# Performance work log

Hardware: AMD Instinct MI355X
Metric: run time of the kernel (lower is better)

The kernel has to match this reference:

```python
import jax, jax.numpy as jnp
import numpy as np

EMBED_DIM = 1024
NUM_HEADS = 16
HEAD_DIM = EMBED_DIM // NUM_HEADS


def setup_inputs() -> dict:
    key = jax.random.key(0)
    k1, k2, k3 = jax.random.split(key, 3)
    B, S = 2, 2048
    x = jax.random.normal(k1, (B, S, EMBED_DIM), dtype=jnp.float32)
    # Xavier-uniform-style init for dense kernels
    lim_qkv = float(np.sqrt(6.0 / (EMBED_DIM + 3 * EMBED_DIM)))
    w_qkv = jax.random.uniform(k2, (EMBED_DIM, 3 * EMBED_DIM), jnp.float32, -lim_qkv, lim_qkv)
    b_qkv = jnp.zeros((3 * EMBED_DIM,), jnp.float32)
    lim_out = float(np.sqrt(6.0 / (EMBED_DIM + EMBED_DIM)))
    w_out = jax.random.uniform(k3, (EMBED_DIM, EMBED_DIM), jnp.float32, -lim_out, lim_out)
    b_out = jnp.zeros((EMBED_DIM,), jnp.float32)
    return {"x": x, "w_qkv": w_qkv, "b_qkv": b_qkv, "w_out": w_out, "b_out": b_out}


def reference(x, w_qkv, b_qkv, w_out, b_out):
    B, S, E = x.shape
    qkv = x @ w_qkv + b_qkv                       # [B, S, 3E]
    qkv = qkv.reshape(B, S, NUM_HEADS, 3 * HEAD_DIM)
    qkv = qkv.transpose(0, 2, 1, 3)               # [B, H, S, 3*dh]
    q, k, v = jnp.split(qkv, 3, axis=-1)          # each [B, H, S, dh]
    scale = 1.0 / jnp.sqrt(jnp.asarray(HEAD_DIM, x.dtype))
    logits = jnp.einsum('bhqd,bhkd->bhqk', q, k) * scale  # [B, H, S, S]
    attn = jax.nn.softmax(logits, axis=-1)
    vals = jnp.einsum('bhqk,bhkd->bhqd', attn, v)  # [B, H, S, dh]
    vals = vals.transpose(0, 2, 1, 3).reshape(B, S, E)
    return vals @ w_out + b_out
```

## Files before the change

### kernel.cpp

```cpp
#include <hip/hip_runtime.h>
#include <cstdint>

typedef unsigned short u16;
typedef unsigned int u32;
typedef __attribute__((ext_vector_type(8))) short bf16x8;
typedef __attribute__((ext_vector_type(4))) float f32x4;

#if __has_builtin(__builtin_amdgcn_exp2f)
#define EXP2(x) __builtin_amdgcn_exp2f(x)
#else
#define EXP2(x) exp2f(x)
#endif

__device__ __forceinline__ u16 f2bf(float f) {
  unsigned u = __float_as_uint(f);
  u += 0x7fffu + ((u >> 16) & 1u);
  return (u16)(u >> 16);
}
__device__ __forceinline__ u32 pk_bf16(float lo, float hi) {
#if __has_builtin(__builtin_amdgcn_cvt_pk_bf16_f32)
  auto r = __builtin_amdgcn_cvt_pk_bf16_f32(lo, hi);
  return __builtin_bit_cast(u32, r);
#else
  u32 a = __float_as_uint(lo), b = __float_as_uint(hi);
  a += 0x7fffu + ((a >> 16) & 1u);
  b += 0x7fffu + ((b >> 16) & 1u);
  return (a >> 16) | (b & 0xffff0000u);
#endif
}

__device__ __forceinline__ void async_load16(const void* g, void* l) {
  typedef const __attribute__((address_space(1))) void* gp_t;
  typedef __attribute__((address_space(3))) void* lp_t;
  __builtin_amdgcn_global_load_lds((gp_t)(uintptr_t)g, (lp_t)(uintptr_t)l, 16, 0, 0);
}

__global__ __launch_bounds__(256) void cvt_f32_bf16(
    const float* __restrict__ src, u16* __restrict__ dst)
{
  const size_t i = ((size_t)blockIdx.x * 256 + threadIdx.x) * 8;
  const float4 a = *(const float4*)(src + i);
  const float4 b = *(const float4*)(src + i + 4);
  union { u16 u[8]; bf16x8 v; } p;
  p.u[0] = f2bf(a.x); p.u[1] = f2bf(a.y); p.u[2] = f2bf(a.z); p.u[3] = f2bf(a.w);
  p.u[4] = f2bf(b.x); p.u[5] = f2bf(b.y); p.u[6] = f2bf(b.z); p.u[7] = f2bf(b.w);
  *(bf16x8*)(dst + i) = p.v;
}

__global__ __launch_bounds__(256) void transpose_cvt(
    const float* __restrict__ src, u16* __restrict__ dst, int rows, int cols)
{
  __shared__ u16 tile[64][65];
  const int t = threadIdx.x;
  const int r = t >> 2, c0 = (t & 3) * 16;
  const int tr = blockIdx.y * 64, tc = blockIdx.x * 64;
  const float* sp = src + (size_t)(tr + r) * cols + tc + c0;
#pragma unroll
  for (int i = 0; i < 16; i += 4) {
    const float4 v = *(const float4*)(sp + i);
    tile[r][c0 + i + 0] = f2bf(v.x);
    tile[r][c0 + i + 1] = f2bf(v.y);
    tile[r][c0 + i + 2] = f2bf(v.z);
    tile[r][c0 + i + 3] = f2bf(v.w);
  }
  __syncthreads();
  u16* dp = dst + (size_t)(tc + r) * rows + tr + c0;
#pragma unroll
  for (int i = 0; i < 16; ++i) dp[i] = tile[c0 + i][r];
}

__global__ __launch_bounds__(256) void transpose_v(
    const u16* __restrict__ src, u16* __restrict__ dst)
{
  __shared__ u16 tile[64][72];
  const int t = threadIdx.x;
  const int r = t >> 2, c0 = (t & 3) * 16;
  const int bh = blockIdx.y, s0 = blockIdx.x * 64;
  const u16* sp = src + ((size_t)bh * 2048 + s0 + r) * 64 + c0;
  union { u16 u[8]; bf16x8 v; } a, b;
  a.v = *(const bf16x8*)sp;
  b.v = *(const bf16x8*)(sp + 8);
#pragma unroll
  for (int i = 0; i < 8; ++i) tile[r][c0 + i] = a.u[i];
#pragma unroll
  for (int i = 0; i < 8; ++i) tile[r][c0 + 8 + i] = b.u[i];
  __syncthreads();
  union { u16 u[8]; bf16x8 v; } x, y;
#pragma unroll
  for (int i = 0; i < 8; ++i) x.u[i] = tile[c0 + i][r];
#pragma unroll
  for (int i = 0; i < 8; ++i) y.u[i] = tile[c0 + 8 + i][r];
  u16* dp = dst + ((size_t)bh * 64 + r) * 2048 + s0 + c0;
  *(bf16x8*)dp = x.v;
  *(bf16x8*)(dp + 8) = y.v;
}

__global__ __launch_bounds__(256) void gemm_qkv(
    const u16* __restrict__ A, const u16* __restrict__ Bt, const float* __restrict__ bias,
    u16* __restrict__ Qp, u16* __restrict__ Kp, u16* __restrict__ Vp, int Kd)
{
  __shared__ __align__(16) u16 As[128 * 32];
  __shared__ __align__(16) u16 Bs[128 * 32];
  const int t = threadIdx.x;
  const int lane = t & 63, wave = t >> 6;
  const int quad = lane >> 4, m16 = lane & 15;
  const int mb = blockIdx.y * 128, nb = blockIdx.x * 128;
  const int wr = (wave & 1) * 64, wc = (wave >> 1) * 64;

  const int srow = t >> 2;
  const int scol = (t & 3) * 8;
  const u16* Ag0 = A + (size_t)(mb + srow) * Kd + scol;
  const u16* Ag1 = Ag0 + (size_t)64 * Kd;
  const u16* Bg0 = Bt + (size_t)(nb + srow) * Kd + scol;
  const u16* Bg1 = Bg0 + (size_t)64 * Kd;
  u16* AsD = As + t * 8;
  u16* BsD = Bs + t * 8;

  f32x4 acc[4][4] = {};

  for (int k0 = 0; k0 < Kd; k0 += 32) {
    __syncthreads();
    async_load16(Ag0 + k0, AsD);
    async_load16(Ag1 + k0, AsD + 2048);
    async_load16(Bg0 + k0, BsD);
    async_load16(Bg1 + k0, BsD + 2048);
    __syncthreads();
    bf16x8 af[4], bfr[4];
#pragma unroll
    for (int i = 0; i < 4; ++i)
      af[i] = *(const bf16x8*)(As + (wr + i * 16 + m16) * 32 + quad * 8);
#pragma unroll
    for (int i = 0; i < 4; ++i)
      bfr[i] = *(const bf16x8*)(Bs + (wc + i * 16 + m16) * 32 + quad * 8);
#pragma unroll
    for (int i = 0; i < 4; ++i)
#pragma unroll
      for (int j = 0; j < 4; ++j)
        acc[i][j] = __builtin_amdgcn_mfma_f32_16x16x32_bf16(af[i], bfr[j], acc[i][j], 0, 0, 0);
  }

#pragma unroll
  for (int j = 0; j < 4; ++j) {
    const int base = nb + wc + j * 16;
    const float bv = bias[base + m16];
    const int seg = base >> 6;
    const int h = seg / 3;
    const int which = seg - h * 3;
    const int d = (base & 63) + m16;
    const float qs = (which == 0) ? 0.18033688011112042f : 1.0f;
#pragma unroll
    for (int i = 0; i < 4; ++i)
#pragma unroll
      for (int r = 0; r < 4; ++r) {
        const int row = mb + wr + i * 16 + quad * 4 + r;
        const int b = row >> 11, sI = row & 2047;
        const u16 v = f2bf((acc[i][j][r] + bv) * qs);
        const size_t idx = (((size_t)((b << 4) | h)) * 2048 + sI) * 64 + d;
        if (which == 0)      Qp[idx] = v;
        else if (which == 1) Kp[idx] = v;
        else                 Vp[idx] = v;
      }
  }
}

__global__ __launch_bounds__(256) void gemm_out(
    const u16* __restrict__ A, const u16* __restrict__ Bt, const float* __restrict__ bias,
    float* __restrict__ Outp)
{
  const int Kd = 1024;
  __shared__ __align__(16) u16 As[64 * 32];
  __shared__ __align__(16) u16 Bs[128 * 32];
  const int t = threadIdx.x;
  const int lane = t & 63, wave = t >> 6;
  const int quad = lane >> 4, m16 = lane & 15;
  const int mb = blockIdx.y * 64, nb = blockIdx.x * 128;
  const int wr = (wave & 1) * 32, wc = (wave >> 1) * 64;

  const int srow = t >> 2;
  const int scol = (t & 3) * 8;
  const u16* Ag0 = A + (size_t)(mb + srow) * Kd + scol;
  const u16* Bg0 = Bt + (size_t)(nb + srow) * Kd + scol;
  const u16* Bg1 = Bg0 + (size_t)64 * Kd;
  u16* AsD = As + t * 8;
  u16* BsD = Bs + t * 8;

  f32x4 acc[2][4] = {};

  for (int k0 = 0; k0 < Kd; k0 += 32) {
    __syncthreads();
    async_load16(Ag0 + k0, AsD);
    async_load16(Bg0 + k0, BsD);
    async_load16(Bg1 + k0, BsD + 2048);
    __syncthreads();
    bf16x8 af[2], bfr[4];
#pragma unroll
    for (int i = 0; i < 2; ++i)
      af[i] = *(const bf16x8*)(As + (wr + i * 16 + m16) * 32 + quad * 8);
#pragma unroll
    for (int j = 0; j < 4; ++j)
      bfr[j] = *(const bf16x8*)(Bs + (wc + j * 16 + m16) * 32 + quad * 8);
#pragma unroll
    for (int i = 0; i < 2; ++i)
#pragma unroll
      for (int j = 0; j < 4; ++j)
        acc[i][j] = __builtin_amdgcn_mfma_f32_16x16x32_bf16(af[i], bfr[j], acc[i][j], 0, 0, 0);
  }

#pragma unroll
  for (int j = 0; j < 4; ++j) {
    const int col = nb + wc + j * 16 + m16;
    const float bv = bias[col];
#pragma unroll
    for (int i = 0; i < 2; ++i)
#pragma unroll
      for (int r = 0; r < 4; ++r) {
        const int row = mb + wr + i * 16 + quad * 4 + r;
        Outp[(size_t)row * 1024 + col] = acc[i][j][r] + bv;
      }
  }
}

__global__ __launch_bounds__(256) void flash_attn(
    const u16* __restrict__ Q, const u16* __restrict__ K, const u16* __restrict__ Vt,
    u16* __restrict__ O)
{
  const int S = 2048;
  __shared__ __align__(16) u16 Kl[2][64 * 64];
  __shared__ __align__(16) u16 Vl[2][64 * 64];
  __shared__ __align__(16) u32 Pl[4][16 * 32];
  const int t = threadIdx.x;
  const int lane = t & 63, w = t >> 6;
  const int quad = lane >> 4, m16 = lane & 15;

  const int f = blockIdx.x;
  const int wi = f >> 3;
  const int bh = (f & 7) + 8 * (wi & 3);
  const int q0 = (wi >> 2) * 64;

  const u16* Qb = Q + (size_t)bh * S * 64;
  const u16* Kb = K + (size_t)bh * S * 64;
  const u16* Vb = Vt + (size_t)bh * 64 * S;

  bf16x8 qf[2];
#pragma unroll
  for (int ks = 0; ks < 2; ++ks)
    qf[ks] = *(const bf16x8*)(Qb + (size_t)(q0 + w * 16 + m16) * 64 + ks * 32 + quad * 8);

  const u16* Kg[2]; const u16* Vg[2]; int soff[2];
#pragma unroll
  for (int l = 0; l < 2; ++l) {
    const int idx = l * 256 + t;
    const int row = idx >> 3, slot = idx & 7;
    const int sg = slot ^ (row & 7);
    Kg[l] = Kb + row * 64 + sg * 8;
    Vg[l] = Vb + (size_t)row * S + sg * 8;
    soff[l] = idx * 8;
  }

  f32x4 ot[4] = {};
  f32x4 lr4 = {0.f, 0.f, 0.f, 0.f};
  u32* const Pw = &Pl[w][0];

#pragma unroll
  for (int l = 0; l < 2; ++l) async_load16(Kg[l], &Kl[0][soff[l]]);
#pragma unroll
  for (int l = 0; l < 2; ++l) async_load16(Vg[l], &Vl[0][soff[l]]);
  __syncthreads();

  int buf = 0;
  for (int kv0 = 0; kv0 < S; kv0 += 64, buf ^= 1) {
    if (kv0 + 64 < S) {
      const int nb = buf ^ 1;
#pragma unroll
      for (int l = 0; l < 2; ++l) async_load16(Kg[l] + (kv0 + 64) * 64, &Kl[nb][soff[l]]);
#pragma unroll
      for (int l = 0; l < 2; ++l) async_load16(Vg[l] + (kv0 + 64), &Vl[nb][soff[l]]);
    }
    const u16* Klc = Kl[buf];
    const u16* Vlc = Vl[buf];

    f32x4 st[4] = {};
#pragma unroll
    for (int nt = 0; nt < 4; ++nt) {
      const int j = nt * 16 + m16;
      const u16* rowp = Klc + j * 64;
      const bf16x8 kb0 = *(const bf16x8*)(rowp + ((quad ^ (j & 7)) * 8));
      const bf16x8 kb1 = *(const bf16x8*)(rowp + (((4 + quad) ^ (j & 7)) * 8));
      st[nt] = __builtin_amdgcn_mfma_f32_16x16x32_bf16(kb0, qf[0], st[nt], 0, 0, 0);
      st[nt] = __builtin_amdgcn_mfma_f32_16x16x32_bf16(kb1, qf[1], st[nt], 0, 0, 0);
    }

#pragma unroll
    for (int nt = 0; nt < 4; ++nt) {
      f32x4 p;
#pragma unroll
      for (int r = 0; r < 4; ++r) p[r] = EXP2(st[nt][r]);
      lr4 += p;
      const u32 lo = pk_bf16(p[0], p[1]);
      const u32 hi = pk_bf16(p[2], p[3]);
      const int gp = (2 * nt + (quad >> 1)) ^ (m16 & 7);
      u32* dst = Pw + m16 * 32 + gp * 4 + (quad & 1) * 2;
      *(uint2*)dst = make_uint2(lo, hi);
    }

#pragma unroll
    for (int ks = 0; ks < 2; ++ks) {
      const int pg = (ks * 4 + quad) ^ (m16 & 7);
      const bf16x8 pb = *(const bf16x8*)(Pw + m16 * 32 + pg * 4);
#pragma unroll
      for (int dt = 0; dt < 4; ++dt) {
        const int d = dt * 16 + m16;
        const bf16x8 va = *(const bf16x8*)(Vlc + d * 64 + (((ks * 4 + quad) ^ (d & 7)) * 8));
        ot[dt] = __builtin_amdgcn_mfma_f32_16x16x32_bf16(va, pb, ot[dt], 0, 0, 0);
      }
    }

    __syncthreads();
  }

  float l = lr4[0] + lr4[1] + lr4[2] + lr4[3];
  l += __shfl_xor(l, 16, 64);
  l += __shfl_xor(l, 32, 64);
  const float inv = 1.0f / l;
  const int b = bh >> 4, h = bh & 15;
  const int q = q0 + w * 16 + m16;
  u16* base = O + ((size_t)b * 2048 + q) * 1024 + h * 64;
#pragma unroll
  for (int dt = 0; dt < 4; ++dt) {
    const u32 lo = pk_bf16(ot[dt][0] * inv, ot[dt][1] * inv);
    const u32 hi = pk_bf16(ot[dt][2] * inv, ot[dt][3] * inv);
    *(uint2*)(base + dt * 16 + quad * 4) = make_uint2(lo, hi);
  }
}

extern "C" void kernel_launch(void* const* d_in, const int* in_sizes, int n_in,
                              void* d_out, int out_size, void* d_ws, size_t ws_size,
                              hipStream_t stream)
{
  const float* x     = (const float*)d_in[0];
  const float* w_qkv = (const float*)d_in[1];
  const float* b_qkv = (const float*)d_in[2];
  const float* w_out = (const float*)d_in[3];
  const float* b_out = (const float*)d_in[4];
  float* out = (float*)d_out;

  u16* ws     = (u16*)d_ws;
  u16* xb     = ws;
  u16* WtQKV  = xb + 4194304;
  u16* WtOut  = WtQKV + 3145728;
  u16* Qm     = WtOut + 1048576;
  u16* Km     = Qm + 4194304;
  u16* Vtm    = Km + 4194304;
  u16* AO     = Vtm + 4194304;
  u16* Vm     = AO;

  cvt_f32_bf16<<<2048, 256, 0, stream>>>(x, xb);
  transpose_cvt<<<dim3(48, 16), 256, 0, stream>>>(w_qkv, WtQKV, 1024, 3072);
  transpose_cvt<<<dim3(16, 16), 256, 0, stream>>>(w_out, WtOut, 1024, 1024);
  gemm_qkv<<<dim3(24, 32), 256, 0, stream>>>(xb, WtQKV, b_qkv, Qm, Km, Vm, 1024);
  transpose_v<<<dim3(32, 32), 256, 0, stream>>>(Vm, Vtm);
  flash_attn<<<1024, 256, 0, stream>>>(Qm, Km, Vtm, AO);
  gemm_out<<<dim3(8, 64), 256, 0, stream>>>(AO, WtOut, b_out, out);
}
```

Before: 204.7 us.

## Double query rows per attention block and merge weight transpose launches

Each flash attention block now handles 128 queries (32 per wave, in two 16-row groups) instead of 64, so every K/V tile loaded into LDS is reused across twice as many MFMAs. The grid is halved to 512 blocks. The KV loop is unrolled by two with explicit double-buffer steps, which removes the runtime buffer index. The two weight transpose-convert launches are merged into one kernel to save a launch. In exchange, register pressure rises from the doubled accumulators, and the smaller grid may leave some compute units idle.

After: 202.7 us. No clear change (-1.0%).

```diff
diff --git a/kernel.cpp b/kernel.cpp
--- a/kernel.cpp
+++ b/kernel.cpp
@@ -47,13 +47,20 @@
   *(bf16x8*)(dst + i) = p.v;
 }
 
-__global__ __launch_bounds__(256) void transpose_cvt(
-    const float* __restrict__ src, u16* __restrict__ dst, int rows, int cols)
+__global__ __launch_bounds__(256) void transpose_cvt2(
+    const float* __restrict__ wqkv, u16* __restrict__ dqkv,
+    const float* __restrict__ wout, u16* __restrict__ dout)
 {
   __shared__ u16 tile[64][65];
   const int t = threadIdx.x;
   const int r = t >> 2, c0 = (t & 3) * 16;
-  const int tr = blockIdx.y * 64, tc = blockIdx.x * 64;
+  const bool isOut = blockIdx.x >= 48;
+  const float* src = isOut ? wout : wqkv;
+  u16* dst = isOut ? dout : dqkv;
+  const int cols = isOut ? 1024 : 3072;
+  const int rows = 1024;
+  const int tc = (isOut ? (blockIdx.x - 48) : blockIdx.x) * 64;
+  const int tr = blockIdx.y * 64;
   const float* sp = src + (size_t)(tr + r) * cols + tc + c0;
 #pragma unroll
   for (int i = 0; i < 16; i += 4) {
@@ -227,7 +234,7 @@
   const int S = 2048;
   __shared__ __align__(16) u16 Kl[2][64 * 64];
   __shared__ __align__(16) u16 Vl[2][64 * 64];
-  __shared__ __align__(16) u32 Pl[4][16 * 32];
+  __shared__ __align__(16) u32 Pl[4][2][16 * 32];
   const int t = threadIdx.x;
   const int lane = t & 63, w = t >> 6;
   const int quad = lane >> 4, m16 = lane & 15;
@@ -235,16 +242,18 @@
   const int f = blockIdx.x;
   const int wi = f >> 3;
   const int bh = (f & 7) + 8 * (wi & 3);
-  const int q0 = (wi >> 2) * 64;
+  const int q0 = (wi >> 2) * 128;
 
   const u16* Qb = Q + (size_t)bh * S * 64;
   const u16* Kb = K + (size_t)bh * S * 64;
   const u16* Vb = Vt + (size_t)bh * 64 * S;
 
-  bf16x8 qf[2];
-#pragma unroll
-  for (int ks = 0; ks < 2; ++ks)
-    qf[ks] = *(const bf16x8*)(Qb + (size_t)(q0 + w * 16 + m16) * 64 + ks * 32 + quad * 8);
+  bf16x8 qf[2][2];
+#pragma unroll
+  for (int g = 0; g < 2; ++g)
+#pragma unroll
+    for (int ks = 0; ks < 2; ++ks)
+      qf[g][ks] = *(const bf16x8*)(Qb + (size_t)(q0 + w * 32 + g * 16 + m16) * 64 + ks * 32 + quad * 8);
 
   const u16* Kg[2]; const u16* Vg[2]; int soff[2];
 #pragma unroll
@@ -257,79 +266,93 @@
     soff[l] = idx * 8;
   }
 
-  f32x4 ot[4] = {};
-  f32x4 lr4 = {0.f, 0.f, 0.f, 0.f};
-  u32* const Pw = &Pl[w][0];
-
-#pragma unroll
-  for (int l = 0; l < 2; ++l) async_load16(Kg[l], &Kl[0][soff[l]]);
-#pragma unroll
-  for (int l = 0; l < 2; ++l) async_load16(Vg[l], &Vl[0][soff[l]]);
+  f32x4 ot[2][4] = {};
+  f32x4 lr4[2] = {{0.f,0.f,0.f,0.f},{0.f,0.f,0.f,0.f}};
+  u32* const Pw0 = &Pl[w][0][0];
+  u32* const Pw1 = &Pl[w][1][0];
+
+#define PREFETCH(kvp, B)                                                     \
+  do {                                                                       \
+    _Pragma("unroll")                                                        \
+    for (int l = 0; l < 2; ++l) async_load16(Kg[l] + (kvp) * 64, &Kl[B][soff[l]]); \
+    _Pragma("unroll")                                                        \
+    for (int l = 0; l < 2; ++l) async_load16(Vg[l] + (kvp), &Vl[B][soff[l]]);      \
+  } while (0)
+
+#define STEP(B)                                                              \
+  do {                                                                       \
+    f32x4 st[2][4] = {};                                                     \
+    _Pragma("unroll")                                                        \
+    for (int nt = 0; nt < 4; ++nt) {                                         \
+      const int j = nt * 16 + m16;                                           \
+      const u16* rowp = &Kl[B][j * 64];                                      \
+      const bf16x8 kb0 = *(const bf16x8*)(rowp + ((quad ^ (j & 7)) * 8));    \
+      const bf16x8 kb1 = *(const bf16x8*)(rowp + (((4 + quad) ^ (j & 7)) * 8)); \
+      st[0][nt] = __builtin_amdgcn_mfma_f32_16x16x32_bf16(kb0, qf[0][0], st[0][nt], 0, 0, 0); \
+      st[1][nt] = __builtin_amdgcn_mfma_f32_16x16x32_bf16(kb0, qf[1][0], st[1][nt], 0, 0, 0); \
+      st[0][nt] = __builtin_amdgcn_mfma_f32_16x16x32_bf16(kb1, qf[0][1], st[0][nt], 0, 0, 0); \
+      st[1][nt] = __builtin_amdgcn_mfma_f32_16x16x32_bf16(kb1, qf[1][1], st[1][nt], 0, 0, 0); \
+    }                                                                        \
+    _Pragma("unroll")                                                        \
+    for (int g = 0; g < 2; ++g) {                                            \
+      u32* const Pw = g ? Pw1 : Pw0;                                         \
+      _Pragma("unroll")                                                      \
+      for (int nt = 0; nt < 4; ++nt) {                                       \
+        f32x4 p;                                                             \
+        _Pragma("unroll")                                                    \
+        for (int r = 0; r < 4; ++r) p[r] = EXP2(st[g][nt][r]);               \
+        lr4[g] += p;                                                         \
+        const u32 lo = pk_bf16(p[0], p[1]);                                  \
+        const u32 hi = pk_bf16(p[2], p[3]);                                  \
+        const int gp = (2 * nt + (quad >> 1)) ^ (m16 & 7);                   \
+        u32* dst = Pw + m16 * 32 + gp * 4 + (quad & 1) * 2;                  \
+        *(uint2*)dst = make_uint2(lo, hi);                                   \
+      }                                                                      \
+    }                                                                        \
+    _Pragma("unroll")                                                        \
+    for (int ks = 0; ks < 2; ++ks) {                                         \
+      const int pg = (ks * 4 + quad) ^ (m16 & 7);                            \
+      const bf16x8 pb0 = *(const bf16x8*)(Pw0 + m16 * 32 + pg * 4);          \
+      const bf16x8 pb1 = *(const bf16x8*)(Pw1 + m16 * 32 + pg * 4);          \
+      _Pragma("unroll")                                                      \
+      for (int dt = 0; dt < 4; ++dt) {                                       \
+        const int d = dt * 16 + m16;                                         \
+        const bf16x8 va = *(const bf16x8*)(&Vl[B][d * 64] + (((ks * 4 + quad) ^ (d & 7)) * 8)); \
+        ot[0][dt] = __builtin_amdgcn_mfma_f32_16x16x32_bf16(va, pb0, ot[0][dt], 0, 0, 0); \
+        ot[1][dt] = __builtin_amdgcn_mfma_f32_16x16x32_bf16(va, pb1, ot[1][dt], 0, 0, 0); \
+      }                                                                      \
+    }                                                                        \
+  } while (0)
+
+  PREFETCH(0, 0);
   __syncthreads();
 
-  int buf = 0;
-  for (int kv0 = 0; kv0 < S; kv0 += 64, buf ^= 1) {
-    if (kv0 + 64 < S) {
-      const int nb = buf ^ 1;
-#pragma unroll
-      for (int l = 0; l < 2; ++l) async_load16(Kg[l] + (kv0 + 64) * 64, &Kl[nb][soff[l]]);
-#pragma unroll
-      for (int l = 0; l < 2; ++l) async_load16(Vg[l] + (kv0 + 64), &Vl[nb][soff[l]]);
+  for (int kv0 = 0; kv0 < S; kv0 += 128) {
+    PREFETCH(kv0 + 64, 1);
+    STEP(0);
+    __syncthreads();
+    if (kv0 + 128 < S) PREFETCH(kv0 + 128, 0);
+    STEP(1);
+    __syncthreads();
+  }
+#undef PREFETCH
+#undef STEP
+
+  const int b = bh >> 4, h = bh & 15;
+#pragma unroll
+  for (int g = 0; g < 2; ++g) {
+    float l = lr4[g][0] + lr4[g][1] + lr4[g][2] + lr4[g][3];
+    l += __shfl_xor(l, 16, 64);
+    l += __shfl_xor(l, 32, 64);
+    const float inv = 1.0f / l;
+    const int q = q0 + w * 32 + g * 16 + m16;
+    u16* base = O + ((size_t)b * 2048 + q) * 1024 + h * 64;
+#pragma unroll
+    for (int dt = 0; dt < 4; ++dt) {
+      const u32 lo = pk_bf16(ot[g][dt][0] * inv, ot[g][dt][1] * inv);
+      const u32 hi = pk_bf16(ot[g][dt][2] * inv, ot[g][dt][3] * inv);
+      *(uint2*)(base + dt * 16 + quad * 4) = make_uint2(lo, hi);
     }
-    const u16* Klc = Kl[buf];
-    const u16* Vlc = Vl[buf];
-
-    f32x4 st[4] = {};
-#pragma unroll
-    for (int nt = 0; nt < 4; ++nt) {
-      const int j = nt * 16 + m16;
-      const u16* rowp = Klc + j * 64;
-      const bf16x8 kb0 = *(const bf16x8*)(rowp + ((quad ^ (j & 7)) * 8));
-      const bf16x8 kb1 = *(const bf16x8*)(rowp + (((4 + quad) ^ (j & 7)) * 8));
-      st[nt] = __builtin_amdgcn_mfma_f32_16x16x32_bf16(kb0, qf[0], st[nt], 0, 0, 0);
-      st[nt] = __builtin_amdgcn_mfma_f32_16x16x32_bf16(kb1, qf[1], st[nt], 0, 0, 0);
-    }
-
-#pragma unroll
-    for (int nt = 0; nt < 4; ++nt) {
-      f32x4 p;
-#pragma unroll
-      for (int r = 0; r < 4; ++r) p[r] = EXP2(st[nt][r]);
-      lr4 += p;
-      const u32 lo = pk_bf16(p[0], p[1]);
-      const u32 hi = pk_bf16(p[2], p[3]);
-      const int gp = (2 * nt + (quad >> 1)) ^ (m16 & 7);
-      u32* dst = Pw + m16 * 32 + gp * 4 + (quad & 1) * 2;
-      *(uint2*)dst = make_uint2(lo, hi);
-    }
-
-#pragma unroll
-    for (int ks = 0; ks < 2; ++ks) {
-      const int pg = (ks * 4 + quad) ^ (m16 & 7);
-      const bf16x8 pb = *(const bf16x8*)(Pw + m16 * 32 + pg * 4);
-#pragma unroll
-      for (int dt = 0; dt < 4; ++dt) {
-        const int d = dt * 16 + m16;
-        const bf16x8 va = *(const bf16x8*)(Vlc + d * 64 + (((ks * 4 + quad) ^ (d & 7)) * 8));
-        ot[dt] = __builtin_amdgcn_mfma_f32_16x16x32_bf16(va, pb, ot[dt], 0, 0, 0);
-      }
-    }
-
-    __syncthreads();
-  }
-
-  float l = lr4[0] + lr4[1] + lr4[2] + lr4[3];
-  l += __shfl_xor(l, 16, 64);
-  l += __shfl_xor(l, 32, 64);
-  const float inv = 1.0f / l;
-  const int b = bh >> 4, h = bh & 15;
-  const int q = q0 + w * 16 + m16;
-  u16* base = O + ((size_t)b * 2048 + q) * 1024 + h * 64;
-#pragma unroll
-  for (int dt = 0; dt < 4; ++dt) {
-    const u32 lo = pk_bf16(ot[dt][0] * inv, ot[dt][1] * inv);
-    const u32 hi = pk_bf16(ot[dt][2] * inv, ot[dt][3] * inv);
-    *(uint2*)(base + dt * 16 + quad * 4) = make_uint2(lo, hi);
   }
 }
 
@@ -355,10 +378,9 @@
   u16* Vm     = AO;
 
   cvt_f32_bf16<<<2048, 256, 0, stream>>>(x, xb);
-  transpose_cvt<<<dim3(48, 16), 256, 0, stream>>>(w_qkv, WtQKV, 1024, 3072);
-  transpose_cvt<<<dim3(16, 16), 256, 0, stream>>>(w_out, WtOut, 1024, 1024);
+  transpose_cvt2<<<dim3(64, 16), 256, 0, stream>>>(w_qkv, WtQKV, w_out, WtOut);
   gemm_qkv<<<dim3(24, 32), 256, 0, stream>>>(xb, WtQKV, b_qkv, Qm, Km, Vm, 1024);
   transpose_v<<<dim3(32, 32), 256, 0, stream>>>(Vm, Vtm);
-  flash_attn<<<1024, 256, 0, stream>>>(Qm, Km, Vtm, AO);
+  flash_attn<<<512, 256, 0, stream>>>(Qm, Km, Vtm, AO);
   gemm_out<<<dim3(8, 64), 256, 0, stream>>>(AO, WtOut, b_out, out);
 }
```
